# Kernel optimization log

Measured on AMD Instinct MI355X. Metric: run time of the kernel, lower is better.

Reference implementation:

```python
import jax, jax.numpy as jnp
import numpy as np

NU, NI, E, H, L = 200000, 100000, 1000000, 128, 2


def setup_inputs() -> dict:
    key = jax.random.key(0)
    ks = jax.random.split(key, 16)
    inp = {
        "x_user": jax.random.normal(ks[0], (NU, 32), jnp.float32),
        "x_item": jax.random.normal(ks[1], (NI, 64), jnp.float32),
        "user_lin_w": jax.random.normal(ks[2], (32, H), jnp.float32) / np.sqrt(32.0),
        "user_lin_b": jax.random.normal(ks[3], (H,), jnp.float32) * 0.01,
        "item_lin_w": jax.random.normal(ks[4], (64, H), jnp.float32) / np.sqrt(64.0),
        "item_lin_b": jax.random.normal(ks[5], (H,), jnp.float32) * 0.01,
        # [layer, edge_type] with edge_type 0 = user->item (dst item), 1 = item->user (dst user)
        "conv_wl": jax.random.normal(ks[6], (L, 2, H, H), jnp.float32) / np.sqrt(float(H)),
        "conv_bl": jax.random.normal(ks[7], (L, 2, H), jnp.float32) * 0.01,
        "conv_wr": jax.random.normal(ks[8], (L, 2, H, H), jnp.float32) / np.sqrt(float(H)),
        "src_u2i": jax.random.randint(ks[9], (E,), 0, NU, jnp.int64),
        "dst_u2i": jax.random.randint(ks[10], (E,), 0, NI, jnp.int64),
        "src_i2u": jax.random.randint(ks[11], (E,), 0, NI, jnp.int64),
        "dst_i2u": jax.random.randint(ks[12], (E,), 0, NU, jnp.int64),
    }
    return inp


def _mean_agg(x_src, src, dst, num_dst):
    # gather neighbor features along edges, scatter-mean onto destinations
    msg = x_src[src]  # [E, H]
    s = jax.ops.segment_sum(msg, dst, num_segments=num_dst)
    cnt = jax.ops.segment_sum(jnp.ones((src.shape[0], 1), x_src.dtype), dst, num_segments=num_dst)
    return s / jnp.maximum(cnt, 1.0)


def reference(x_user, x_item, user_lin_w, user_lin_b, item_lin_w, item_lin_b,
              conv_wl, conv_bl, conv_wr, src_u2i, dst_u2i, src_i2u, dst_i2u):
    # type-specific input projections
    u = x_user @ user_lin_w + user_lin_b  # [NU, H]
    i = x_item @ item_lin_w + item_lin_b  # [NI, H]
    num_u, num_i = u.shape[0], i.shape[0]
    for l in range(conv_wl.shape[0]):
        # SAGEConv per edge type: lin_l(mean_agg(x_src)) + lin_r(x_dst)
        agg_i = _mean_agg(u, src_u2i, dst_u2i, num_i)
        agg_u = _mean_agg(i, src_i2u, dst_i2u, num_u)
        new_i = agg_i @ conv_wl[l, 0] + conv_bl[l, 0] + i @ conv_wr[l, 0]
        new_u = agg_u @ conv_wl[l, 1] + conv_bl[l, 1] + u @ conv_wr[l, 1]
        u = jax.nn.relu(new_u)
        i = jax.nn.relu(new_i)
    return (u, i)
```

## Files before the change

### kernel.cpp

```cpp
#include <hip/hip_runtime.h>

#define HF 128

typedef __attribute__((ext_vector_type(8))) short short8;
typedef __attribute__((ext_vector_type(16))) float f32x16;

__device__ inline unsigned short f2bf(float x) {
  unsigned u = __float_as_uint(x);
  unsigned r = u + 0x7fffu + ((u >> 16) & 1u);
  return (unsigned short)(r >> 16);
}

__device__ inline void split8(const float4 fa, const float4 fb, short8& hi, short8& lo)
{
  float f[8] = {fa.x, fa.y, fa.z, fa.w, fb.x, fb.y, fb.z, fb.w};
  union { unsigned int u[4]; short8 s; } H, L;
#pragma unroll
  for (int p = 0; p < 4; ++p) {
    unsigned u0 = __float_as_uint(f[2 * p]);
    unsigned u1 = __float_as_uint(f[2 * p + 1]);
    H.u[p] = (u0 >> 16) | (u1 & 0xffff0000u);
    float l0 = f[2 * p]     - __uint_as_float(u0 & 0xffff0000u);
    float l1 = f[2 * p + 1] - __uint_as_float(u1 & 0xffff0000u);
    L.u[p] = (unsigned)f2bf(l0) | ((unsigned)f2bf(l1) << 16);
  }
  hi = H.s; lo = L.s;
}

template<int K>
__global__ __launch_bounds__(256) void proj_kernel(
    const float* __restrict__ x, const float* __restrict__ w,
    const float* __restrict__ b, float* __restrict__ out, int N)
{
  __shared__ float w_s[K][HF];
  __shared__ float x_s[64][K];
  const int tid = threadIdx.x;
  const int r0 = blockIdx.x * 64;

  for (int idx = tid; idx < K * (HF / 4); idx += 256) {
    int k = idx >> 5, c4 = idx & 31;
    *(float4*)&w_s[k][c4 * 4] = *(const float4*)(w + (size_t)k * HF + c4 * 4);
  }
  for (int idx = tid; idx < 64 * (K / 4); idx += 256) {
    int r = idx / (K / 4), c4 = idx % (K / 4);
    int row = r0 + r;
    float4 v = {0.f, 0.f, 0.f, 0.f};
    if (row < N) v = *(const float4*)(x + (size_t)row * K + c4 * 4);
    *(float4*)&x_s[r][c4 * 4] = v;
  }
  __syncthreads();

  const int cg = tid & 31;
  const int rg = tid >> 5;
  const int jc = cg * 4;
  const float4 bv = *(const float4*)(b + jc);
  float acc[8][4];
#pragma unroll
  for (int rr = 0; rr < 8; ++rr) {
    acc[rr][0] = bv.x; acc[rr][1] = bv.y; acc[rr][2] = bv.z; acc[rr][3] = bv.w;
  }

  for (int k = 0; k < K; k += 4) {
    float4 wv[4];
#pragma unroll
    for (int t = 0; t < 4; ++t) wv[t] = *(const float4*)&w_s[k + t][jc];
#pragma unroll
    for (int rr = 0; rr < 8; ++rr) {
      const float4 x4 = *(const float4*)&x_s[rg * 8 + rr][k];
      float xa[4] = {x4.x, x4.y, x4.z, x4.w};
#pragma unroll
      for (int t = 0; t < 4; ++t) {
        acc[rr][0] = fmaf(xa[t], wv[t].x, acc[rr][0]);
        acc[rr][1] = fmaf(xa[t], wv[t].y, acc[rr][1]);
        acc[rr][2] = fmaf(xa[t], wv[t].z, acc[rr][2]);
        acc[rr][3] = fmaf(xa[t], wv[t].w, acc[rr][3]);
      }
    }
  }

#pragma unroll
  for (int rr = 0; rr < 8; ++rr) {
    int row = r0 + rg * 8 + rr;
    if (row < N) {
      float4 o = {acc[rr][0], acc[rr][1], acc[rr][2], acc[rr][3]};
      *(float4*)(out + (size_t)row * HF + jc) = o;
    }
  }
}

__global__ void count_kernel(const int* __restrict__ dst, int* __restrict__ cnt,
                             int* __restrict__ pos, int E)
{
  int e = blockIdx.x * blockDim.x + threadIdx.x;
  if (e < E) pos[e] = atomicAdd(&cnt[dst[e]], 1);
}

__global__ __launch_bounds__(1024) void scan_p1(int* __restrict__ data, int* __restrict__ bsum, int n)
{
  __shared__ int s[1024];
  int tid = threadIdx.x;
  int i = blockIdx.x * 1024 + tid;
  int v = (i < n) ? data[i] : 0;
  s[tid] = v;
  __syncthreads();
  for (int off = 1; off < 1024; off <<= 1) {
    int t = (tid >= off) ? s[tid - off] : 0;
    __syncthreads();
    s[tid] += t;
    __syncthreads();
  }
  if (i < n) data[i] = s[tid] - v;
  if (tid == 1023) bsum[blockIdx.x] = s[1023];
}

__global__ __launch_bounds__(1024) void scan_p2(int* __restrict__ bsum, int nb)
{
  __shared__ int s[1024];
  int tid = threadIdx.x;
  int v = (tid < nb) ? bsum[tid] : 0;
  s[tid] = v;
  __syncthreads();
  for (int off = 1; off < 1024; off <<= 1) {
    int t = (tid >= off) ? s[tid - off] : 0;
    __syncthreads();
    s[tid] += t;
    __syncthreads();
  }
  if (tid < nb) bsum[tid] = s[tid] - v;
}

__global__ __launch_bounds__(1024) void scan_p3(int* __restrict__ data, const int* __restrict__ bsum,
                                                int n, int total)
{
  int i = blockIdx.x * 1024 + threadIdx.x;
  if (i < n) data[i] += bsum[blockIdx.x];
  if (i == 0) data[n] = total;
}

__global__ void fill_kernel(const int* __restrict__ dst, const int* __restrict__ src,
                            const int* __restrict__ rp, const int* __restrict__ pos,
                            int* __restrict__ colv, int E)
{
  int e = blockIdx.x * blockDim.x + threadIdx.x;
  if (e < E) colv[rp[dst[e]] + pos[e]] = src[e];
}

__global__ __launch_bounds__(256) void agg_kernel(
    const float* __restrict__ feat, const int* __restrict__ rp,
    const int* __restrict__ colv, float* __restrict__ out, int ndst)
{
  int gw = (int)((blockIdx.x * blockDim.x + threadIdx.x) >> 6);
  int lane = threadIdx.x & 63;
  int half = lane >> 5;
  int fi = (lane & 31) * 4;
  int nw = (int)((gridDim.x * blockDim.x) >> 6);
  for (int d = gw; d < ndst; d += nw) {
    int beg = rp[d], end = rp[d + 1];
    float4 a0 = {0.f, 0.f, 0.f, 0.f}, a1 = {0.f, 0.f, 0.f, 0.f};
    int j = beg + half;
    for (; j + 2 < end; j += 4) {
      int s0 = colv[j];
      int s1 = colv[j + 2];
      const float4 v0 = *(const float4*)(feat + (size_t)s0 * HF + fi);
      const float4 v1 = *(const float4*)(feat + (size_t)s1 * HF + fi);
      a0.x += v0.x; a0.y += v0.y; a0.z += v0.z; a0.w += v0.w;
      a1.x += v1.x; a1.y += v1.y; a1.z += v1.z; a1.w += v1.w;
    }
    for (; j < end; j += 2) {
      int s0 = colv[j];
      const float4 v0 = *(const float4*)(feat + (size_t)s0 * HF + fi);
      a0.x += v0.x; a0.y += v0.y; a0.z += v0.z; a0.w += v0.w;
    }
    float4 a;
    a.x = a0.x + a1.x; a.y = a0.y + a1.y; a.z = a0.z + a1.z; a.w = a0.w + a1.w;
    a.x += __shfl_xor(a.x, 32);
    a.y += __shfl_xor(a.y, 32);
    a.z += __shfl_xor(a.z, 32);
    a.w += __shfl_xor(a.w, 32);
    if (half == 0) {
      int dg = end - beg;
      float inv = 1.0f / (float)(dg > 0 ? dg : 1);
      float4 o = {a.x * inv, a.y * inv, a.z * inv, a.w * inv};
      *(float4*)(out + (size_t)d * HF + fi) = o;
    }
  }
}

__global__ void wpack_kernel(const float* __restrict__ wl, const float* __restrict__ wr,
                             unsigned char* __restrict__ bpack, int ncombo)
{
  int t = blockIdx.x * 256 + threadIdx.x;
  int total = ncombo << 12;
  if (t >= total) return;
  int lane = t & 63;
  int ct = (t >> 6) & 3;
  int kt = (t >> 8) & 1;
  int kc = (t >> 9) & 7;
  int combo = t >> 12;
  const float* WL = wl + (size_t)combo * HF * HF;
  const float* WR = wr + (size_t)combo * HF * HF;
  int col = ct * 32 + (lane & 31);
  int kbase = kc * 32 + kt * 16 + (lane >> 5) * 8;
  float f[8];
#pragma unroll
  for (int j = 0; j < 8; ++j) {
    int k = kbase + j;
    f[j] = (k < HF) ? WL[(size_t)k * HF + col] : WR[(size_t)(k - HF) * HF + col];
  }
  unsigned int hi[4], lo[4];
#pragma unroll
  for (int p = 0; p < 4; ++p) {
    unsigned u0 = __float_as_uint(f[2 * p]);
    unsigned u1 = __float_as_uint(f[2 * p + 1]);
    hi[p] = (u0 >> 16) | (u1 & 0xffff0000u);
    float l0 = f[2 * p]     - __uint_as_float(u0 & 0xffff0000u);
    float l1 = f[2 * p + 1] - __uint_as_float(u1 & 0xffff0000u);
    lo[p] = (unsigned)f2bf(l0) | ((unsigned)f2bf(l1) << 16);
  }
  size_t base = (size_t)combo * 131072 + kc * 16384 + kt * 4096 + ct * 1024 + lane * 16;
  uint4 h = {hi[0], hi[1], hi[2], hi[3]};
  uint4 l = {lo[0], lo[1], lo[2], lo[3]};
  *(uint4*)(bpack + base) = h;
  *(uint4*)(bpack + base + 8192) = l;
}

__global__ __launch_bounds__(256) void sage_mfma(
    const float* __restrict__ agg, const float* __restrict__ x,
    const unsigned char* __restrict__ bpk, const float* __restrict__ bias,
    float* __restrict__ out, int N)
{
  __shared__ float4 a_s4[2][1024];
  const int tid = threadIdx.x;
  const int lane = tid & 63;
  const int w = tid >> 6;
  const int wr_ = w >> 1;
  const int wc  = w & 1;
  const int r0 = blockIdx.x * 128;

  float4 areg[4];

  f32x16 acc[2][2];
#pragma unroll
  for (int a = 0; a < 2; ++a)
#pragma unroll
    for (int b = 0; b < 2; ++b)
#pragma unroll
      for (int i = 0; i < 16; ++i) acc[a][b][i] = 0.f;

  {
    const int colbase = 0;
#pragma unroll
    for (int i = 0; i < 4; ++i) {
      int idx = i * 256 + tid;
      int r = idx >> 3, c = idx & 7;
      int grow = r0 + r;
      float4 v = {0.f, 0.f, 0.f, 0.f};
      if (grow < N) v = *(const float4*)(agg + (size_t)grow * HF + colbase + c * 4);
      areg[i] = v;
    }
#pragma unroll
    for (int i = 0; i < 4; ++i) {
      int idx = i * 256 + tid;
      int r = idx >> 3, c = idx & 7;
      a_s4[0][r * 8 + (c ^ (r & 7))] = areg[i];
    }
  }

  int cur = 0;
  for (int kc = 0; kc < 8; ++kc) {
    __syncthreads();

    if (kc < 7) {
      const float* srcp = (kc + 1 < 4) ? agg : x;
      const int colbase = ((kc + 1) & 3) * 32;
#pragma unroll
      for (int i = 0; i < 4; ++i) {
        int idx = i * 256 + tid;
        int r = idx >> 3, c = idx & 7;
        int grow = r0 + r;
        float4 v = {0.f, 0.f, 0.f, 0.f};
        if (grow < N) v = *(const float4*)(srcp + (size_t)grow * HF + colbase + c * 4);
        areg[i] = v;
      }
    }

    const uint4* gb = (const uint4*)(bpk + (size_t)kc * 16384);
    union U { uint4 u; short8 s; } bhi[2][2], blo[2][2];
#pragma unroll
    for (int kt = 0; kt < 2; ++kt)
#pragma unroll
      for (int ctl = 0; ctl < 2; ++ctl) {
        int ct = wc * 2 + ctl;
        int fi = kt * 256 + ct * 64 + lane;
        bhi[kt][ctl].u = gb[fi];
        blo[kt][ctl].u = gb[512 + fi];
      }

#pragma unroll
    for (int kt = 0; kt < 2; ++kt) {
      short8 ahi[2], alo[2];
#pragma unroll
      for (int rt = 0; rt < 2; ++rt) {
        int row_l = wr_ * 64 + rt * 32 + (lane & 31);
        int c0 = kt * 4 + (lane >> 5) * 2;
        float4 fa = a_s4[cur][row_l * 8 + (c0 ^ (row_l & 7))];
        float4 fb = a_s4[cur][row_l * 8 + ((c0 + 1) ^ (row_l & 7))];
        split8(fa, fb, ahi[rt], alo[rt]);
      }
#pragma unroll
      for (int rt = 0; rt < 2; ++rt)
#pragma unroll
        for (int ctl = 0; ctl < 2; ++ctl) {
          acc[rt][ctl] = __builtin_amdgcn_mfma_f32_32x32x16_bf16(ahi[rt], bhi[kt][ctl].s, acc[rt][ctl], 0, 0, 0);
          acc[rt][ctl] = __builtin_amdgcn_mfma_f32_32x32x16_bf16(ahi[rt], blo[kt][ctl].s, acc[rt][ctl], 0, 0, 0);
          acc[rt][ctl] = __builtin_amdgcn_mfma_f32_32x32x16_bf16(alo[rt], bhi[kt][ctl].s, acc[rt][ctl], 0, 0, 0);
        }
    }

    if (kc < 7) {
#pragma unroll
      for (int i = 0; i < 4; ++i) {
        int idx = i * 256 + tid;
        int r = idx >> 3, c = idx & 7;
        a_s4[cur ^ 1][r * 8 + (c ^ (r & 7))] = areg[i];
      }
    }
    cur ^= 1;
  }

#pragma unroll
  for (int ctl = 0; ctl < 2; ++ctl) {
    int gcol = wc * 64 + ctl * 32 + (lane & 31);
    float bv = bias[gcol];
#pragma unroll
    for (int rt = 0; rt < 2; ++rt) {
#pragma unroll
      for (int reg = 0; reg < 16; ++reg) {
        int row_l = (reg & 3) + 8 * (reg >> 2) + 4 * (lane >> 5);
        int grow = r0 + wr_ * 64 + rt * 32 + row_l;
        if (grow < N) {
          float v = acc[rt][ctl][reg] + bv;
          out[(size_t)grow * HF + gcol] = fmaxf(v, 0.f);
        }
      }
    }
  }
}

extern "C" void kernel_launch(void* const* d_in, const int* in_sizes, int n_in,
                              void* d_out, int out_size, void* d_ws, size_t ws_size,
                              hipStream_t stream)
{
  const float* x_user  = (const float*)d_in[0];
  const float* x_item  = (const float*)d_in[1];
  const float* user_w  = (const float*)d_in[2];
  const float* user_b  = (const float*)d_in[3];
  const float* item_w  = (const float*)d_in[4];
  const float* item_b  = (const float*)d_in[5];
  const float* conv_wl = (const float*)d_in[6];
  const float* conv_bl = (const float*)d_in[7];
  const float* conv_wr = (const float*)d_in[8];
  const int* src_u2i = (const int*)d_in[9];
  const int* dst_u2i = (const int*)d_in[10];
  const int* src_i2u = (const int*)d_in[11];
  const int* dst_i2u = (const int*)d_in[12];

  const int NU = in_sizes[0] / 32;
  const int NI = in_sizes[1] / 64;
  const int E  = in_sizes[9];
  const int L  = in_sizes[6] / (2 * HF * HF);

  float* out_u = (float*)d_out;
  float* out_i = out_u + (size_t)NU * HF;

  char* wsb = (char*)d_ws;
  size_t off = 0;
  auto alloc = [&](size_t bytes) -> void* {
    void* p = wsb + off;
    off = (off + bytes + 255) & ~(size_t)255;
    return p;
  };
  float* uA    = (float*)alloc((size_t)NU * HF * 4);
  float* iA    = (float*)alloc((size_t)NI * HF * 4);
  float* agg_u = (float*)alloc((size_t)NU * HF * 4);
  float* agg_i = (float*)alloc((size_t)NI * HF * 4);
  int* rp_i    = (int*)alloc((size_t)(NI + 1) * 4);
  int* rp_u    = (int*)alloc((size_t)(NU + 1) * 4);
  int* pos     = (int*)alloc((size_t)E * 4);
  int* col_u2i = (int*)alloc((size_t)E * 4);
  int* col_i2u = (int*)alloc((size_t)E * 4);
  int* bsum    = (int*)alloc(4096 * 4);
  unsigned char* bpack = (unsigned char*)alloc((size_t)(2 * L) * 131072);
  (void)ws_size; (void)n_in; (void)out_size;

  proj_kernel<32><<<(NU + 63) / 64, 256, 0, stream>>>(x_user, user_w, user_b, out_u, NU);
  proj_kernel<64><<<(NI + 63) / 64, 256, 0, stream>>>(x_item, item_w, item_b, out_i, NI);

  {
    int total = (2 * L) << 12;
    wpack_kernel<<<(total + 255) / 256, 256, 0, stream>>>(conv_wl, conv_wr, bpack, 2 * L);
  }

  auto build_csr = [&](const int* dst, const int* srcv, int* rp, int* colv, int n) {
    (void)hipMemsetAsync(rp, 0, (size_t)(n + 1) * sizeof(int), stream);
    int gE = (E + 255) / 256;
    count_kernel<<<gE, 256, 0, stream>>>(dst, rp, pos, E);
    int nb = (n + 1023) / 1024;
    scan_p1<<<nb, 1024, 0, stream>>>(rp, bsum, n);
    scan_p2<<<1, 1024, 0, stream>>>(bsum, nb);
    scan_p3<<<nb, 1024, 0, stream>>>(rp, bsum, n, E);
    fill_kernel<<<gE, 256, 0, stream>>>(dst, srcv, rp, pos, colv, E);
  };
  build_csr(dst_u2i, src_u2i, rp_i, col_u2i, NI);
  build_csr(dst_i2u, src_i2u, rp_u, col_i2u, NU);

  const float* cu = out_u;
  const float* ci = out_i;
  for (int l = 0; l < L; ++l) {
    float* nu = (l & 1) ? out_u : uA;
    float* ni = (l & 1) ? out_i : iA;

    agg_kernel<<<(NI + 3) / 4, 256, 0, stream>>>(cu, rp_i, col_u2i, agg_i, NI);
    agg_kernel<<<(NU + 3) / 4, 256, 0, stream>>>(ci, rp_u, col_i2u, agg_u, NU);

    const unsigned char* bp0 = bpack + (size_t)(l * 2 + 0) * 131072;
    const unsigned char* bp1 = bpack + (size_t)(l * 2 + 1) * 131072;
    const float* bl0 = conv_bl + (size_t)(l * 2 + 0) * HF;
    const float* bl1 = conv_bl + (size_t)(l * 2 + 1) * HF;

    sage_mfma<<<(NI + 127) / 128, 256, 0, stream>>>(agg_i, ci, bp0, bl0, ni, NI);
    sage_mfma<<<(NU + 127) / 128, 256, 0, stream>>>(agg_u, cu, bp1, bl1, nu, NU);

    cu = nu;
    ci = ni;
  }
}
```

Measured before the change: 1.080 ms.

## Drop LDS staging in SAGE MFMA kernel and load A fragments from global

Rewrites the dense SAGE projection kernel so each wave loads its A-operand fragments directly from global memory into registers instead of staging them through double-buffered shared memory with barriers. The block tile shrinks from 128 to 64 rows, with each wave covering 32 rows by 64 columns, and the grid doubles to match. This removes LDS traffic, __syncthreads and swizzle overhead and lowers register use per wave, which may raise occupancy. In exchange each row is read by two waves (both column halves), and the B fragments are re-fetched from global per wave with less reuse per row.

```diff
diff --git a/kernel.cpp b/kernel.cpp
--- a/kernel.cpp
+++ b/kernel.cpp
@@ -224,124 +224,78 @@
   *(uint4*)(bpack + base + 8192) = l;
 }
 
+union BU { uint4 u; short8 s; };
+
 __global__ __launch_bounds__(256) void sage_mfma(
     const float* __restrict__ agg, const float* __restrict__ x,
     const unsigned char* __restrict__ bpk, const float* __restrict__ bias,
     float* __restrict__ out, int N)
 {
-  __shared__ float4 a_s4[2][1024];
   const int tid = threadIdx.x;
   const int lane = tid & 63;
   const int w = tid >> 6;
-  const int wr_ = w >> 1;
-  const int wc  = w & 1;
-  const int r0 = blockIdx.x * 128;
-
-  float4 areg[4];
-
-  f32x16 acc[2][2];
-#pragma unroll
-  for (int a = 0; a < 2; ++a)
-#pragma unroll
-    for (int b = 0; b < 2; ++b)
-#pragma unroll
-      for (int i = 0; i < 16; ++i) acc[a][b][i] = 0.f;
-
-  {
-    const int colbase = 0;
-#pragma unroll
-    for (int i = 0; i < 4; ++i) {
-      int idx = i * 256 + tid;
-      int r = idx >> 3, c = idx & 7;
-      int grow = r0 + r;
-      float4 v = {0.f, 0.f, 0.f, 0.f};
-      if (grow < N) v = *(const float4*)(agg + (size_t)grow * HF + colbase + c * 4);
-      areg[i] = v;
-    }
-#pragma unroll
-    for (int i = 0; i < 4; ++i) {
-      int idx = i * 256 + tid;
-      int r = idx >> 3, c = idx & 7;
-      a_s4[0][r * 8 + (c ^ (r & 7))] = areg[i];
-    }
-  }
-
-  int cur = 0;
+  const int wrow = w >> 1;
+  const int wcol = w & 1;
+  const int rbase = blockIdx.x * 64 + wrow * 32;
+  const int row = rbase + (lane & 31);
+  const bool rok = row < N;
+  const int khalf = (lane >> 5) * 8;
+
+  f32x16 acc[2];
+#pragma unroll
+  for (int c = 0; c < 2; ++c)
+#pragma unroll
+    for (int i = 0; i < 16; ++i) acc[c][i] = 0.f;
+
+#pragma unroll
   for (int kc = 0; kc < 8; ++kc) {
-    __syncthreads();
-
-    if (kc < 7) {
-      const float* srcp = (kc + 1 < 4) ? agg : x;
-      const int colbase = ((kc + 1) & 3) * 32;
-#pragma unroll
-      for (int i = 0; i < 4; ++i) {
-        int idx = i * 256 + tid;
-        int r = idx >> 3, c = idx & 7;
-        int grow = r0 + r;
-        float4 v = {0.f, 0.f, 0.f, 0.f};
-        if (grow < N) v = *(const float4*)(srcp + (size_t)grow * HF + colbase + c * 4);
-        areg[i] = v;
-      }
+    const float* srcp = (kc < 4) ? agg : x;
+    const int cb = (kc & 3) * 32;
+
+    short8 ahi[2], alo[2];
+#pragma unroll
+    for (int kt = 0; kt < 2; ++kt) {
+      float4 fa = {0.f, 0.f, 0.f, 0.f}, fb = {0.f, 0.f, 0.f, 0.f};
+      if (rok) {
+        const float* p = srcp + (size_t)row * HF + cb + kt * 16 + khalf;
+        fa = *(const float4*)p;
+        fb = *(const float4*)(p + 4);
+      }
+      split8(fa, fb, ahi[kt], alo[kt]);
     }
 
     const uint4* gb = (const uint4*)(bpk + (size_t)kc * 16384);
-    union U { uint4 u; short8 s; } bhi[2][2], blo[2][2];
+    BU bhi[2][2], blo[2][2];
 #pragma unroll
     for (int kt = 0; kt < 2; ++kt)
 #pragma unroll
-      for (int ctl = 0; ctl < 2; ++ctl) {
-        int ct = wc * 2 + ctl;
-        int fi = kt * 256 + ct * 64 + lane;
-        bhi[kt][ctl].u = gb[fi];
-        blo[kt][ctl].u = gb[512 + fi];
-      }
-
-#pragma unroll
-    for (int kt = 0; kt < 2; ++kt) {
-      short8 ahi[2], alo[2];
-#pragma unroll
-      for (int rt = 0; rt < 2; ++rt) {
-        int row_l = wr_ * 64 + rt * 32 + (lane & 31);
-        int c0 = kt * 4 + (lane >> 5) * 2;
-        float4 fa = a_s4[cur][row_l * 8 + (c0 ^ (row_l & 7))];
-        float4 fb = a_s4[cur][row_l * 8 + ((c0 + 1) ^ (row_l & 7))];
-        split8(fa, fb, ahi[rt], alo[rt]);
-      }
-#pragma unroll
-      for (int rt = 0; rt < 2; ++rt)
-#pragma unroll
-        for (int ctl = 0; ctl < 2; ++ctl) {
-          acc[rt][ctl] = __builtin_amdgcn_mfma_f32_32x32x16_bf16(ahi[rt], bhi[kt][ctl].s, acc[rt][ctl], 0, 0, 0);
-          acc[rt][ctl] = __builtin_amdgcn_mfma_f32_32x32x16_bf16(ahi[rt], blo[kt][ctl].s, acc[rt][ctl], 0, 0, 0);
-          acc[rt][ctl] = __builtin_amdgcn_mfma_f32_32x32x16_bf16(alo[rt], bhi[kt][ctl].s, acc[rt][ctl], 0, 0, 0);
-        }
-    }
-
-    if (kc < 7) {
-#pragma unroll
-      for (int i = 0; i < 4; ++i) {
-        int idx = i * 256 + tid;
-        int r = idx >> 3, c = idx & 7;
-        a_s4[cur ^ 1][r * 8 + (c ^ (r & 7))] = areg[i];
-      }
-    }
-    cur ^= 1;
-  }
-
-#pragma unroll
-  for (int ctl = 0; ctl < 2; ++ctl) {
-    int gcol = wc * 64 + ctl * 32 + (lane & 31);
+      for (int ct = 0; ct < 2; ++ct) {
+        int fi = kt * 256 + (wcol * 2 + ct) * 64 + lane;
+        bhi[kt][ct].u = gb[fi];
+        blo[kt][ct].u = gb[512 + fi];
+      }
+
+#pragma unroll
+    for (int kt = 0; kt < 2; ++kt)
+#pragma unroll
+      for (int ct = 0; ct < 2; ++ct) {
+        acc[ct] = __builtin_amdgcn_mfma_f32_32x32x16_bf16(ahi[kt], bhi[kt][ct].s, acc[ct], 0, 0, 0);
+        acc[ct] = __builtin_amdgcn_mfma_f32_32x32x16_bf16(ahi[kt], blo[kt][ct].s, acc[ct], 0, 0, 0);
+        acc[ct] = __builtin_amdgcn_mfma_f32_32x32x16_bf16(alo[kt], bhi[kt][ct].s, acc[ct], 0, 0, 0);
+      }
+  }
+
+#pragma unroll
+  for (int ct = 0; ct < 2; ++ct) {
+    int gcol = wcol * 64 + ct * 32 + (lane & 31);
     float bv = bias[gcol];
 #pragma unroll
-    for (int rt = 0; rt < 2; ++rt) {
-#pragma unroll
-      for (int reg = 0; reg < 16; ++reg) {
-        int row_l = (reg & 3) + 8 * (reg >> 2) + 4 * (lane >> 5);
-        int grow = r0 + wr_ * 64 + rt * 32 + row_l;
-        if (grow < N) {
-          float v = acc[rt][ctl][reg] + bv;
-          out[(size_t)grow * HF + gcol] = fmaxf(v, 0.f);
-        }
+    for (int reg = 0; reg < 16; ++reg) {
+      int row_l = (reg & 3) + 8 * (reg >> 2) + 4 * (lane >> 5);
+      int grow = rbase + row_l;
+      if (grow < N) {
+        float v = acc[ct][reg] + bv;
+        out[(size_t)grow * HF + gcol] = fmaxf(v, 0.f);
       }
     }
   }
@@ -428,8 +382,8 @@
     const float* bl0 = conv_bl + (size_t)(l * 2 + 0) * HF;
     const float* bl1 = conv_bl + (size_t)(l * 2 + 1) * HF;
 
-    sage_mfma<<<(NI + 127) / 128, 256, 0, stream>>>(agg_i, ci, bp0, bl0, ni, NI);
-    sage_mfma<<<(NU + 127) / 128, 256, 0, stream>>>(agg_u, cu, bp1, bl1, nu, NU);
+    sage_mfma<<<(NI + 63) / 64, 256, 0, stream>>>(agg_i, ci, bp0, bl0, ni, NI);
+    sage_mfma<<<(NU + 63) / 64, 256, 0, stream>>>(agg_u, cu, bp1, bl1, nu, NU);
 
     cu = nu;
     ci = ni;
```

After: 1.128 ms. 4.4% more time.
